# Performance work log

Hardware: AMD Instinct MI355X
Metric: run time of the kernel (lower is better)

## Reference

```python
import jax, jax.numpy as jnp
import numpy as np

B, C, H, W = 1, 512, 64, 64
HEADS, DIM_HEAD = 8, 64
GROUPS = 32
EPS = 1e-5
SCALE = DIM_HEAD ** -0.5


def setup_inputs() -> dict:
    key = jax.random.key(0)
    ks = jax.random.split(key, 8)
    inner = HEADS * DIM_HEAD  # 512
    s = 0.02
    return {
        "hidden_states": jax.random.normal(ks[0], (B, C, H, W), jnp.float32),
        "gn_gamma": jnp.ones((C,), jnp.float32),
        "gn_beta": jnp.zeros((C,), jnp.float32),
        "wq": jax.random.normal(ks[1], (inner, C), jnp.float32) * s,
        "wk": jax.random.normal(ks[2], (inner, C), jnp.float32) * s,
        "wv": jax.random.normal(ks[3], (inner, C), jnp.float32) * s,
        "wo": jax.random.normal(ks[4], (C, inner), jnp.float32) * s,
        "bo": jnp.zeros((C,), jnp.float32),
    }


def _group_norm(x, gamma, beta):
    # x: [B, C, H, W]; normalize within channel groups over (C//G, H, W)
    b, c, h, w = x.shape
    xg = x.reshape(b, GROUPS, c // GROUPS, h, w)
    mean = xg.mean(axis=(2, 3, 4), keepdims=True)
    var = xg.var(axis=(2, 3, 4), keepdims=True)
    xg = (xg - mean) * jax.lax.rsqrt(var + EPS)
    x = xg.reshape(b, c, h, w)
    return x * gamma[None, :, None, None] + beta[None, :, None, None]


def reference(hidden_states, gn_gamma, gn_beta, wq, wk, wv, wo, bo):
    residual = hidden_states
    x = _group_norm(hidden_states, gn_gamma, gn_beta)
    b, c, h, w = x.shape
    n = h * w
    x = x.reshape(b, c, n).transpose(0, 2, 1)  # [B, N, C]

    # torch Linear: y = x @ W^T (bias=False for q/k/v)
    q = (x @ wq.T).reshape(b, n, HEADS, DIM_HEAD).transpose(0, 2, 1, 3)  # [B,H,N,D]
    k = (x @ wk.T).reshape(b, n, HEADS, DIM_HEAD).transpose(0, 2, 1, 3)
    v = (x @ wv.T).reshape(b, n, HEADS, DIM_HEAD).transpose(0, 2, 1, 3)

    scores = jnp.einsum("bhqd,bhkd->bhqk", q, k) * SCALE  # [B,H,N,N]
    probs = jax.nn.softmax(scores, axis=-1)
    out = jnp.einsum("bhqk,bhkd->bhqd", probs, v)  # [B,H,N,D]

    out = out.transpose(0, 2, 1, 3).reshape(b, n, HEADS * DIM_HEAD)  # [B,N,inner]
    out = out @ wo.T + bo  # [B,N,C]
    out = out.transpose(0, 2, 1).reshape(b, c, h, w)
    return out + residual
```

## Files before the change

### kernel.cpp

```cpp
#include <hip/hip_runtime.h>

#define N_TOK 4096
#define C_DIM 512
#define NH    8
#define EPS   1e-5f
#define NSPLIT 4

typedef __attribute__((ext_vector_type(8))) __bf16 bf16x8;
typedef __attribute__((ext_vector_type(4))) float  f32x4;
using u16 = unsigned short;
using u32 = unsigned int;

#define MFMA16 __builtin_amdgcn_mfma_f32_16x16x32_bf16

__device__ __forceinline__ u16 f2bf(float f){
  u32 x = __builtin_bit_cast(u32, f);
  x += 0x7fffu + ((x>>16)&1u);
  return (u16)(x>>16);
}
__device__ __forceinline__ float bf2f(u16 v){
  return __builtin_bit_cast(float, (u32)v<<16);
}
__device__ __forceinline__ float exp2a(float x){
  float r; asm("v_exp_f32 %0, %1" : "=v"(r) : "v"(x)); return r;
}
__device__ __forceinline__ u32 cvtpk(float lo, float hi){
  u32 r; asm("v_cvt_pk_bf16_f32 %0, %1, %2" : "=v"(r) : "v"(lo), "v"(hi)); return r;
}
__device__ __forceinline__ float max3a(float a, float b, float c){
  float r; asm("v_max3_f32 %0, %1, %2, %3" : "=v"(r) : "v"(a), "v"(b), "v"(c)); return r;
}
__device__ __forceinline__ void dma16(const void* src, void* lds){
  __builtin_amdgcn_global_load_lds(
      (const __attribute__((address_space(1))) u32*)src,
      (__attribute__((address_space(3))) u32*)lds, 16, 0, 0);
}

__global__ __launch_bounds__(256) void k_pre(const float* __restrict__ s0,
      const float* __restrict__ s1, const float* __restrict__ s2,
      const float* __restrict__ s3, u16* __restrict__ d0, u16* __restrict__ d1,
      u16* __restrict__ d2, u16* __restrict__ d3,
      const float* __restrict__ x, float* __restrict__ pstat,
      u16* __restrict__ xbf){
  __shared__ float rs[4], rss[4];
  int b = blockIdx.x;
  if (b < 1024){
    int m = b >> 8;
    int i = (b & 255)*256 + threadIdx.x;
    const float* s = m==0?s0 : m==1?s1 : m==2?s2 : s3;
    u16*         d = m==0?d0 : m==1?d1 : m==2?d2 : d3;
    float4 v = ((const float4*)s)[i];
    ushort4 o; o.x=f2bf(v.x); o.y=f2bf(v.y); o.z=f2bf(v.z); o.w=f2bf(v.w);
    ((ushort4*)d)[i] = o;
    return;
  }
  int gb = b - 1024;
  int g = gb>>3, p = gb&7, t = threadIdx.x;
  const float4* gx4 = (const float4*)(x + (size_t)g*16*N_TOK) + (size_t)p*2048;
  ushort4* xb4 = (ushort4*)xbf + (size_t)g*16384 + (size_t)p*2048;
  float s=0.f, ss=0.f;
  #pragma unroll
  for (int k=0;k<8;k++){
    float4 v = gx4[t + k*256];
    s  += v.x+v.y+v.z+v.w;
    ss += v.x*v.x+v.y*v.y+v.z*v.z+v.w*v.w;
    ushort4 o; o.x=f2bf(v.x); o.y=f2bf(v.y); o.z=f2bf(v.z); o.w=f2bf(v.w);
    xb4[t + k*256] = o;
  }
  for (int m=1;m<64;m<<=1){ s += __shfl_xor(s,m); ss += __shfl_xor(ss,m); }
  int w=t>>6, lane=t&63;
  if (lane==0){ rs[w]=s; rss[w]=ss; }
  __syncthreads();
  if (t==0){
    pstat[(g*8+p)*2  ] = rs[0]+rs[1]+rs[2]+rs[3];
    pstat[(g*8+p)*2+1] = rss[0]+rss[1]+rss[2]+rss[3];
  }
}

__global__ __launch_bounds__(256) void k_gn_apply(const u16* __restrict__ xbf,
      const float* __restrict__ pstat, const float* __restrict__ gamma,
      const float* __restrict__ beta, u16* __restrict__ X){
  int g = blockIdx.x, c0 = g*16;
  int n = blockIdx.y*256 + threadIdx.x;
  float S=0.f, SS=0.f;
  #pragma unroll
  for (int p=0;p<8;p++){ S += pstat[(g*8+p)*2]; SS += pstat[(g*8+p)*2+1]; }
  float mean = S*(1.f/65536.f);
  float rstd = rsqrtf(SS*(1.f/65536.f) - mean*mean + EPS);
  u16 ov[16];
  #pragma unroll
  for (int c=0;c<16;c++){
    float gm = gamma[c0+c]*rstd;
    float be = beta[c0+c] - mean*gm;
    float v  = bf2f(xbf[(size_t)(c0+c)*N_TOK + n])*gm + be;
    ov[c] = f2bf(v);
  }
  uint4* dst = (uint4*)&X[(size_t)n*C_DIM + c0];
  dst[0] = *(uint4*)&ov[0];
  dst[1] = *(uint4*)&ov[8];
}

__device__ __forceinline__ void gemm_core64(const u16* A, const u16* B,
      int m0, int n0, char* LDS, f32x4 (&acc)[4][2]){
  int t = threadIdx.x, w = t>>6, l = t&63, lr = l&15, li = l>>4;
  int wr = w>>1, wc = w&1;
  char* As = LDS;
  char* Bs = LDS + 32768;
  const char* Ac = (const char*)A + (size_t)m0*1024;
  const char* Bc = (const char*)B + (size_t)n0*1024;
  int rswz = (lr&7)<<4;

  int rowA[4], segA[4], rowB[2], segB[2];
  #pragma unroll
  for (int k=0;k<4;k++){ int s=t+k*256; rowA[k]=s>>3; segA[k]=s&7; }
  #pragma unroll
  for (int k=0;k<2;k++){ int s=t+k*256; rowB[k]=s>>3; segB[k]=s&7; }

  #define STAGE(it, bb) { int koff=(it)*128;                                   \
    _Pragma("unroll")                                                          \
    for (int k=0;k<4;k++){                                                     \
      int ys = (segA[k]*16) ^ ((rowA[k]&7)<<4);                                \
      dma16(Ac + (size_t)rowA[k]*1024 + koff + ys,                             \
            As + (bb)*16384 + w*1024 + k*4096);                                \
    }                                                                          \
    _Pragma("unroll")                                                          \
    for (int k=0;k<2;k++){                                                     \
      int ys = (segB[k]*16) ^ ((rowB[k]&7)<<4);                                \
      dma16(Bc + (size_t)rowB[k]*1024 + koff + ys,                             \
            Bs + (bb)*8192 + w*1024 + k*4096);                                 \
    } }

  STAGE(0, 0);
  __syncthreads();

  int buf = 0;
  for (int it=0; it<8; it++){
    if (it < 7){ STAGE(it+1, buf^1); }
    char* Ab = As + buf*16384;
    char* Bb = Bs + buf*8192;
    #pragma unroll
    for (int ks=0; ks<2; ks++){
      bf16x8 af[4], bfr[2];
      #pragma unroll
      for (int i=0;i<4;i++){
        int ra = wr*64 + i*16 + lr;
        af[i]  = *(const bf16x8*)(Ab + ra*128 + ((li*16 + ks*64) ^ rswz));
      }
      #pragma unroll
      for (int j=0;j<2;j++){
        int rb = wc*32 + j*16 + lr;
        bfr[j] = *(const bf16x8*)(Bb + rb*128 + ((li*16 + ks*64) ^ rswz));
      }
      __builtin_amdgcn_s_setprio(1);
      #pragma unroll
      for (int i=0;i<4;i++){
        #pragma unroll
        for (int j=0;j<2;j++){
          acc[i][j] = MFMA16(af[i], bfr[j], acc[i][j], 0,0,0);
        }
      }
      __builtin_amdgcn_s_setprio(0);
    }
    __syncthreads();
    buf ^= 1;
  }
  #undef STAGE
}

__global__ __launch_bounds__(256,3) void k_qkv2(const u16* __restrict__ X,
      const u16* __restrict__ wq, const u16* __restrict__ wk,
      const u16* __restrict__ wv, u16* __restrict__ Qo, u16* __restrict__ Ko,
      u16* __restrict__ Vto){
  __shared__ char LDS[49152];
  int b = blockIdx.x;
  const u16 *A, *B; u16* Cp; int ldc, m0, n0; float sc = 1.f; bool vperm = false;
  if (b < 256){        A=X;  B=wq; Cp=Qo;  ldc=512;  m0=(b>>3)*128; n0=(b&7)*64;
                       sc = 0.125f*1.44269504f; }
  else if (b < 512){ int r=b-256; A=X;  B=wk; Cp=Ko;  ldc=512;  m0=(r>>3)*128; n0=(r&7)*64; }
  else             { int r=b-512; A=wv; B=X;  Cp=Vto; ldc=4096; m0=(r>>6)*128; n0=(r&63)*64;
                     vperm = true; }

  f32x4 acc[4][2] = {};
  gemm_core64(A, B, m0, n0, LDS, acc);

  int t = threadIdx.x, w = t>>6, l = t&63, lr = l&15, li = l>>4;
  int wr = w>>1, wc = w&1;
  #pragma unroll
  for (int i=0;i<4;i++){
    #pragma unroll
    for (int rr=0;rr<4;rr++){
      int mm = m0 + wr*64 + i*16 + li*4 + rr;
      #pragma unroll
      for (int j=0;j<2;j++){
        int nn = n0 + wc*32 + j*16 + lr;
        if (vperm){
          int tl = nn & 63;
          int pos = (tl & 35) | ((tl & 12) << 1) | ((tl & 16) >> 2);
          nn = (nn & ~63) | pos;
        }
        Cp[(size_t)mm*ldc + nn] = f2bf(acc[i][j][rr]*sc);
      }
    }
  }
}

__global__ __launch_bounds__(256,3) void k_oproj2(const u16* __restrict__ Wo,
      const u16* __restrict__ Ob, const float* __restrict__ bo,
      const float* __restrict__ res, float* __restrict__ out){
  __shared__ char LDS[49152];
  int b = blockIdx.x;
  int m0 = (b>>6)*128, n0 = (b&63)*64;

  f32x4 acc[4][2] = {};
  gemm_core64(Wo, Ob, m0, n0, LDS, acc);

  int t = threadIdx.x, w = t>>6, l = t&63, lr = l&15, li = l>>4;
  int wr = w>>1, wc = w&1;
  #pragma unroll
  for (int i=0;i<4;i++){
    #pragma unroll
    for (int rr=0;rr<4;rr++){
      int cc = m0 + wr*64 + i*16 + li*4 + rr;
      float bias = bo[cc];
      #pragma unroll
      for (int j=0;j<2;j++){
        int nn = n0 + wc*32 + j*16 + lr;
        size_t off = (size_t)cc*4096 + nn;
        out[off] = acc[i][j][rr] + bias + res[off];
      }
    }
  }
}

__global__ __launch_bounds__(256,2) void k_attn12(const u16* __restrict__ Q,
      const u16* __restrict__ K, const u16* __restrict__ Vt,
      u16* __restrict__ Opart, float* __restrict__ ml){
  __shared__ char KV[2][16384];
  int b = blockIdx.x;
  int xcd  = b & 7;
  int slot = b >> 3;
  int pair = xcd*4 + (slot >> 4);
  int h  = pair & 7;
  int sp = pair >> 3;
  int q0 = (slot & 15) * 256;
  int t = threadIdx.x, w = t>>6, l = t&63, lr = l&15, li = l>>4;
  char* KVb = (char*)KV;
  int qbase = q0 + w*64;

  const u16* Qp = Q + (size_t)(qbase + lr)*512 + h*64 + li*8;
  bf16x8 qa[4][2];
  #pragma unroll
  for (int s=0;s<4;s++){
    qa[s][0] = *(const bf16x8*)(Qp + (size_t)s*16*512);
    qa[s][1] = *(const bf16x8*)(Qp + (size_t)s*16*512 + 32);
  }

  int srow = l>>3, y0 = (l&7)*16;
  const char* Kc = (const char*)K;
  const char* Vc = (const char*)Vt;
  const char* ksrc[2]; const char* vsrc[2]; int ldso[2];
  #pragma unroll
  for (int j=0;j<2;j++){
    int row = w*16 + j*8 + srow;
    int ys  = y0 ^ ((row&7)<<4);
    ksrc[j] = Kc + (size_t)(sp*1024 + row)*1024 + h*128 + ys;
    vsrc[j] = Vc + (size_t)(h*64 + row)*8192 + sp*2048 + ys;
    ldso[j] = w*2048 + j*1024;
  }

  #pragma unroll
  for (int j=0;j<2;j++){
    dma16(ksrc[j], KVb + ldso[j]);
    dma16(vsrc[j], KVb + 8192 + ldso[j]);
  }
  __syncthreads();

  f32x4 acc[4][4] = {};
  float lsum[4] = {0.f,0.f,0.f,0.f};
  int buf = 0;

  for (int it=0; it<16; it++){
    if (it < 15){
      int nb = buf^1;
      #pragma unroll
      for (int j=0;j<2;j++){
        dma16(ksrc[j] + (size_t)(it+1)*65536, KVb + nb*16384 + ldso[j]);
        dma16(vsrc[j] + (it+1)*128,           KVb + nb*16384 + 8192 + ldso[j]);
      }
    }
    char* Klb = KVb + buf*16384;
    char* Vlb = Klb + 8192;

    bf16x8 k0[4], k1[4], vf[2][4];
    #pragma unroll
    for (int T=0;T<4;T++){
      int row = T*16 + lr, swz = (row&7)<<4;
      const char* rb = Klb + row*128;
      k0[T] = *(const bf16x8*)(rb + ((li*16     ) ^ swz));
      k1[T] = *(const bf16x8*)(rb + ((li*16 + 64) ^ swz));
      const char* vb = Vlb + row*128;
      vf[0][T] = *(const bf16x8*)(vb + ((     li*16) ^ swz));
      vf[1][T] = *(const bf16x8*)(vb + ((64 + li*16) ^ swz));
    }

    #pragma unroll
    for (int s=0;s<4;s++){
      f32x4 st[4] = {};
      __builtin_amdgcn_s_setprio(1);
      #pragma unroll
      for (int T=0;T<4;T++){
        st[T] = MFMA16(k0[T], qa[s][0], st[T], 0,0,0);
        st[T] = MFMA16(k1[T], qa[s][1], st[T], 0,0,0);
      }
      __builtin_amdgcn_s_setprio(0);

      u32 pk[8];
      float lad = 0.f;
      #pragma unroll
      for (int T=0;T<4;T++){
        float p0=exp2a(st[T][0]), p1=exp2a(st[T][1]);
        float p2=exp2a(st[T][2]), p3=exp2a(st[T][3]);
        lad += (p0+p1)+(p2+p3);
        pk[T*2]   = cvtpk(p0,p1);
        pk[T*2+1] = cvtpk(p2,p3);
      }
      lsum[s] += lad;

      __builtin_amdgcn_s_setprio(1);
      #pragma unroll
      for (int c=0;c<2;c++){
        union { bf16x8 v; u32 u[4]; } A0;
        #pragma unroll
        for (int k=0;k<4;k++){ A0.u[k]=pk[c*4+k]; }
        #pragma unroll
        for (int T=0;T<4;T++){
          acc[s][T] = MFMA16(A0.v, vf[c][T], acc[s][T], 0,0,0);
        }
      }
      __builtin_amdgcn_s_setprio(0);
    }

    __syncthreads();
    buf ^= 1;
  }

  u16* Op = Opart + (size_t)sp*N_TOK*C_DIM;
  #pragma unroll
  for (int s=0;s<4;s++){
    lsum[s] += __shfl_xor(lsum[s],16);
    lsum[s] += __shfl_xor(lsum[s],32);
    #pragma unroll
    for (int T=0;T<4;T++){
      #pragma unroll
      for (int r=0;r<4;r++){
        Op[(size_t)(qbase + s*16 + li*4 + r)*512 + h*64 + T*16 + lr]
            = f2bf(acc[s][T][r]);
      }
    }
    if (li==0){
      float* p0 = ml + (((size_t)sp*NH + h)*N_TOK + qbase + s*16 + lr)*2;
      p0[0]=0.f; p0[1]=lsum[s];
    }
  }
}

__global__ __launch_bounds__(256) void k_merge2(const u16* __restrict__ Opart,
      const float* __restrict__ ml, u16* __restrict__ Ob){
  int i  = blockIdx.x*256 + threadIdx.x;
  int q  = i >> 7;
  int c4 = i & 127;
  int h  = c4 >> 4;
  float m[NSPLIT], lv[NSPLIT];
  #pragma unroll
  for (int s=0;s<NSPLIT;s++){
    const float* p = ml + (((size_t)s*NH + h)*N_TOK + q)*2;
    m[s]=p[0]; lv[s]=p[1];
  }
  float M = fmaxf(max3a(m[0],m[1],m[2]), m[3]);
  float wgt[NSPLIT]; float L = 0.f;
  #pragma unroll
  for (int s=0;s<NSPLIT;s++){ wgt[s] = exp2a(m[s]-M); L += lv[s]*wgt[s]; }
  float inv = 1.f/L;
  float4 o = {0.f,0.f,0.f,0.f};
  #pragma unroll
  for (int s=0;s<NSPLIT;s++){
    ushort4 a = ((const ushort4*)(Opart + (size_t)s*N_TOK*C_DIM))[i];
    o.x += bf2f(a.x)*wgt[s]; o.y += bf2f(a.y)*wgt[s];
    o.z += bf2f(a.z)*wgt[s]; o.w += bf2f(a.w)*wgt[s];
  }
  ushort4 r;
  r.x=f2bf(o.x*inv); r.y=f2bf(o.y*inv); r.z=f2bf(o.z*inv); r.w=f2bf(o.w*inv);
  ((ushort4*)Ob)[i] = r;
}

extern "C" void kernel_launch(void* const* d_in, const int* in_sizes, int n_in,
                              void* d_out, int out_size, void* d_ws, size_t ws_size,
                              hipStream_t stream){
  (void)in_sizes; (void)n_in; (void)out_size; (void)ws_size;
  const float* hs    = (const float*)d_in[0];
  const float* gamma = (const float*)d_in[1];
  const float* beta  = (const float*)d_in[2];
  const float* wq    = (const float*)d_in[3];
  const float* wk    = (const float*)d_in[4];
  const float* wv    = (const float*)d_in[5];
  const float* wo    = (const float*)d_in[6];
  const float* bo    = (const float*)d_in[7];
  float* out = (float*)d_out;

  u16* X   = (u16*)d_ws;
  u16* Qb  = X   + (size_t)4096*512;
  u16* Kb  = Qb  + (size_t)4096*512;
  u16* Vtb = Kb  + (size_t)4096*512;
  u16* Ob  = Vtb + (size_t)4096*512;
  u16* xbf = Ob  + (size_t)4096*512;
  u16* wqb = xbf + (size_t)4096*512;
  u16* wkb = wqb + (size_t)512*512;
  u16* wvb = wkb + (size_t)512*512;
  u16* wob = wvb + (size_t)512*512;
  float* pstat = (float*)(wob + (size_t)512*512);
  u16* Opart   = (u16*)(pstat + 1024);
  float* mlbuf = (float*)(Opart + (size_t)NSPLIT*4096*512);

  k_pre<<<1280,256,0,stream>>>(wq, wk, wv, wo, wqb, wkb, wvb, wob, hs, pstat, xbf);
  dim3 ga(32, 16);
  k_gn_apply<<<ga,256,0,stream>>>(xbf, pstat, gamma, beta, X);
  k_qkv2<<<768,256,0,stream>>>(X, wqb, wkb, wvb, Qb, Kb, Vtb);
  k_attn12<<<512,256,0,stream>>>(Qb, Kb, Vtb, Opart, mlbuf);
  k_merge2<<<2048,256,0,stream>>>(Opart, mlbuf, Ob);
  k_oproj2<<<256,256,0,stream>>>(wob, Ob, bo, hs, out);
}
```

Before: 77.39 us.

## Fuse split-KV merge into output projection GEMM B-operand load

Removes the separate merge kernel and folds the combination of the four split-KV partial outputs into the output projection's B-tile staging. Partials are loaded from global memory, summed, normalised by the summed row sums and written to LDS, so the intermediate Ob round trip and one launch go away. The merge drops the max-based reweighting and relies on the attention kernel writing m=0 for every split. The o-proj now does register loads and ALU merging inside its pipeline, has lower occupancy (launch bounds 2), and computes an unused linv prologue.

```diff
diff --git a/kernel.cpp b/kernel.cpp
--- a/kernel.cpp
+++ b/kernel.cpp
@@ -26,9 +26,6 @@
 }
 __device__ __forceinline__ u32 cvtpk(float lo, float hi){
   u32 r; asm("v_cvt_pk_bf16_f32 %0, %1, %2" : "=v"(r) : "v"(lo), "v"(hi)); return r;
-}
-__device__ __forceinline__ float max3a(float a, float b, float c){
-  float r; asm("v_max3_f32 %0, %1, %2, %3" : "=v"(r) : "v"(a), "v"(b), "v"(c)); return r;
 }
 __device__ __forceinline__ void dma16(const void* src, void* lds){
   __builtin_amdgcn_global_load_lds(
@@ -204,23 +201,126 @@
   }
 }
 
-__global__ __launch_bounds__(256,3) void k_oproj2(const u16* __restrict__ Wo,
-      const u16* __restrict__ Ob, const float* __restrict__ bo,
-      const float* __restrict__ res, float* __restrict__ out){
+__global__ __launch_bounds__(256,2) void k_oproj3(const u16* __restrict__ Wo,
+      const u16* __restrict__ Opart, const float* __restrict__ ml,
+      const float* __restrict__ bo, const float* __restrict__ res,
+      float* __restrict__ out){
   __shared__ char LDS[49152];
   int b = blockIdx.x;
-  int m0 = (b>>6)*128, n0 = (b&63)*64;
-
-  f32x4 acc[4][2] = {};
-  gemm_core64(Wo, Ob, m0, n0, LDS, acc);
-
+  int cm0 = (b>>6)*128, n0 = (b&63)*64;
   int t = threadIdx.x, w = t>>6, l = t&63, lr = l&15, li = l>>4;
   int wr = w>>1, wc = w&1;
+  char* As = LDS;
+  char* Bs = LDS + 32768;
+  const char* Ac = (const char*)Wo + (size_t)cm0*1024;
+  int rswz = (lr&7)<<4;
+
+  int rowA[4], segA[4];
+  #pragma unroll
+  for (int k=0;k<4;k++){ int s=t+k*256; rowA[k]=s>>3; segA[k]=s&7; }
+  int tok[2]; size_t bofs[2]; float linv[2];
+  #pragma unroll
+  for (int k=0;k<2;k++){
+    int s=t+k*256; int row=s>>3; int seg=s&7;
+    tok[k] = n0 + row;
+    bofs[k] = (size_t)tok[k]*1024 + ((seg*16) ^ ((row&7)<<4));
+  }
+  #pragma unroll
+  for (int k=0;k<2;k++){
+    float L = 0.f;
+    #pragma unroll
+    for (int s=0;s<4;s++){
+      L += ml[(((size_t)s*NH + 0)*N_TOK + tok[k])*2 + 1];
+    }
+    linv[k] = L;
+  }
+
+  #define ASTAGE(it, bb) { int koff=(it)*128;                                  \
+    _Pragma("unroll")                                                          \
+    for (int k=0;k<4;k++){                                                     \
+      int ys = (segA[k]*16) ^ ((rowA[k]&7)<<4);                                \
+      dma16(Ac + (size_t)rowA[k]*1024 + koff + ys,                             \
+            As + (bb)*16384 + w*1024 + k*4096);                                \
+    } }
+
+  uint4 pb[2][4];
+  #define BLOAD(hd) {                                                          \
+    _Pragma("unroll")                                                          \
+    for (int k=0;k<2;k++){                                                     \
+      _Pragma("unroll")                                                        \
+      for (int s=0;s<4;s++){                                                   \
+        pb[k][s] = *(const uint4*)((const char*)Opart                          \
+                   + (size_t)s*N_TOK*C_DIM*2 + bofs[k] + (size_t)(hd)*128);    \
+      } } }
+
+  #define BMERGE(hd, bb) {                                                     \
+    _Pragma("unroll")                                                          \
+    for (int k=0;k<2;k++){                                                     \
+      float L = 0.f;                                                           \
+      _Pragma("unroll")                                                        \
+      for (int s=0;s<4;s++){                                                   \
+        L += ml[(((size_t)s*NH + (hd))*N_TOK + tok[k])*2 + 1];                 \
+      }                                                                        \
+      float inv = 1.f/L;                                                       \
+      u16 ob[8];                                                               \
+      const u16* e0=(const u16*)&pb[k][0]; const u16* e1=(const u16*)&pb[k][1];\
+      const u16* e2=(const u16*)&pb[k][2]; const u16* e3=(const u16*)&pb[k][3];\
+      _Pragma("unroll")                                                        \
+      for (int j=0;j<8;j++){                                                   \
+        float v = (bf2f(e0[j])+bf2f(e1[j])) + (bf2f(e2[j])+bf2f(e3[j]));       \
+        ob[j] = f2bf(v*inv);                                                   \
+      }                                                                        \
+      *(uint4*)(Bs + (bb)*8192 + w*1024 + k*4096 + l*16) = *(uint4*)ob;        \
+    } }
+
+  f32x4 acc[4][2] = {};
+
+  ASTAGE(0, 0);
+  BLOAD(0);
+  BMERGE(0, 0);
+  __syncthreads();
+
+  int buf = 0;
+  for (int it=0; it<8; it++){
+    if (it < 7){ ASTAGE(it+1, buf^1); BLOAD(it+1); }
+    char* Ab = As + buf*16384;
+    char* Bb = Bs + buf*8192;
+    #pragma unroll
+    for (int ks=0; ks<2; ks++){
+      bf16x8 af[4], bfr[2];
+      #pragma unroll
+      for (int i=0;i<4;i++){
+        int ra = wr*64 + i*16 + lr;
+        af[i]  = *(const bf16x8*)(Ab + ra*128 + ((li*16 + ks*64) ^ rswz));
+      }
+      #pragma unroll
+      for (int j=0;j<2;j++){
+        int rb = wc*32 + j*16 + lr;
+        bfr[j] = *(const bf16x8*)(Bb + rb*128 + ((li*16 + ks*64) ^ rswz));
+      }
+      __builtin_amdgcn_s_setprio(1);
+      #pragma unroll
+      for (int i=0;i<4;i++){
+        #pragma unroll
+        for (int j=0;j<2;j++){
+          acc[i][j] = MFMA16(af[i], bfr[j], acc[i][j], 0,0,0);
+        }
+      }
+      __builtin_amdgcn_s_setprio(0);
+    }
+    if (it < 7){ BMERGE(it+1, buf^1); }
+    __syncthreads();
+    buf ^= 1;
+  }
+  #undef ASTAGE
+  #undef BLOAD
+  #undef BMERGE
+
   #pragma unroll
   for (int i=0;i<4;i++){
     #pragma unroll
     for (int rr=0;rr<4;rr++){
-      int cc = m0 + wr*64 + i*16 + li*4 + rr;
+      int cc = cm0 + wr*64 + i*16 + li*4 + rr;
       float bias = bo[cc];
       #pragma unroll
       for (int j=0;j<2;j++){
@@ -364,35 +464,6 @@
   }
 }
 
-__global__ __launch_bounds__(256) void k_merge2(const u16* __restrict__ Opart,
-      const float* __restrict__ ml, u16* __restrict__ Ob){
-  int i  = blockIdx.x*256 + threadIdx.x;
-  int q  = i >> 7;
-  int c4 = i & 127;
-  int h  = c4 >> 4;
-  float m[NSPLIT], lv[NSPLIT];
-  #pragma unroll
-  for (int s=0;s<NSPLIT;s++){
-    const float* p = ml + (((size_t)s*NH + h)*N_TOK + q)*2;
-    m[s]=p[0]; lv[s]=p[1];
-  }
-  float M = fmaxf(max3a(m[0],m[1],m[2]), m[3]);
-  float wgt[NSPLIT]; float L = 0.f;
-  #pragma unroll
-  for (int s=0;s<NSPLIT;s++){ wgt[s] = exp2a(m[s]-M); L += lv[s]*wgt[s]; }
-  float inv = 1.f/L;
-  float4 o = {0.f,0.f,0.f,0.f};
-  #pragma unroll
-  for (int s=0;s<NSPLIT;s++){
-    ushort4 a = ((const ushort4*)(Opart + (size_t)s*N_TOK*C_DIM))[i];
-    o.x += bf2f(a.x)*wgt[s]; o.y += bf2f(a.y)*wgt[s];
-    o.z += bf2f(a.z)*wgt[s]; o.w += bf2f(a.w)*wgt[s];
-  }
-  ushort4 r;
-  r.x=f2bf(o.x*inv); r.y=f2bf(o.y*inv); r.z=f2bf(o.z*inv); r.w=f2bf(o.w*inv);
-  ((ushort4*)Ob)[i] = r;
-}
-
 extern "C" void kernel_launch(void* const* d_in, const int* in_sizes, int n_in,
                               void* d_out, int out_size, void* d_ws, size_t ws_size,
                               hipStream_t stream){
@@ -411,8 +482,7 @@
   u16* Qb  = X   + (size_t)4096*512;
   u16* Kb  = Qb  + (size_t)4096*512;
   u16* Vtb = Kb  + (size_t)4096*512;
-  u16* Ob  = Vtb + (size_t)4096*512;
-  u16* xbf = Ob  + (size_t)4096*512;
+  u16* xbf = Vtb + (size_t)4096*512;
   u16* wqb = xbf + (size_t)4096*512;
   u16* wkb = wqb + (size_t)512*512;
   u16* wvb = wkb + (size_t)512*512;
@@ -426,6 +496,5 @@
   k_gn_apply<<<ga,256,0,stream>>>(xbf, pstat, gamma, beta, X);
   k_qkv2<<<768,256,0,stream>>>(X, wqb, wkb, wvb, Qb, Kb, Vtb);
   k_attn12<<<512,256,0,stream>>>(Qb, Kb, Vtb, Opart, mlbuf);
-  k_merge2<<<2048,256,0,stream>>>(Opart, mlbuf, Ob);
-  k_oproj2<<<256,256,0,stream>>>(wob, Ob, bo, hs, out);
-}
+  k_oproj3<<<256,256,0,stream>>>(wob, Opart, mlbuf, bo, hs, out);
+}
```

Result: no change. 78.64 us (+1.6%).
